# Kernel tuning notes

Measured on AMD Instinct MI355X. Metric: run time of the kernel, lower is better.

## Reference

```python
import jax, jax.numpy as jnp
import numpy as np

EPS = 1e-5

def conv3d(x, w):
    # x: [B,C,D,H,W], w: [O,I,3,3,3], stride 1, padding 1 (size preserving)
    return jax.lax.conv_general_dilated(
        x, w, window_strides=(1, 1, 1),
        padding=((1, 1), (1, 1), (1, 1)),
        dimension_numbers=('NCDHW', 'OIDHW', 'NCDHW'))

def deconv3d(x, w):
    # ConvTranspose3d(k=3, s=1, p=1) == conv3d with spatially flipped kernel, in/out swapped
    # torch ConvTranspose3d weight layout: [in, out, kD, kH, kW]
    wc = jnp.flip(w, axis=(2, 3, 4)).transpose(1, 0, 2, 3, 4)
    return conv3d(x, wc)

def batchnorm(x, bn):
    # bn: [4, C] rows = (gamma, beta, running_mean, running_var); inference mode
    g, b, m, v = bn[0], bn[1], bn[2], bn[3]
    scale = g * jax.lax.rsqrt(v + EPS)
    shift = b - m * scale
    return x * scale[None, :, None, None, None] + shift[None, :, None, None, None]

def qrnn_scan(Z, F, reverse):
    # gated linear recurrence h_t = f_t*h_{t-1} + (1-f_t)*z_t over depth axis (dim 2)
    Zs = jnp.moveaxis(Z, 2, 0)  # [D,B,C,H,W]
    Fs = jnp.moveaxis(F, 2, 0)
    def step(h, zf):
        z, f = zf
        h = f * h + (1.0 - f) * z
        return h, h
    h0 = jnp.zeros_like(Zs[0])  # h=None in torch == h=0 since f*0 vanishes
    _, hs = jax.lax.scan(step, h0, (Zs, Fs), reverse=reverse)
    return jnp.moveaxis(hs, 0, 2)

def qrnn_layer(x, w, bn, hidden, reverse, upsample, transpose):
    if upsample:
        # nn.Upsample(scale_factor=(1,2,2)) nearest
        x = jnp.repeat(jnp.repeat(x, 2, axis=3), 2, axis=4)
    g = deconv3d(x, w) if transpose else conv3d(x, w)
    g = batchnorm(g, bn)
    Z, F = g[:, :hidden], g[:, hidden:]
    return qrnn_scan(jnp.tanh(Z), jax.nn.sigmoid(F), reverse)

def setup_inputs():
    key = jax.random.key(0)
    ks = jax.random.split(key, 12)
    B, D = 4, 31
    x = jax.random.normal(ks[0], (B, 64, D, 32, 32), jnp.float32)
    xs2 = jax.random.normal(ks[1], (B, 32, D, 64, 64), jnp.float32)
    xs1 = jax.random.normal(ks[2], (B, 32, D, 64, 64), jnp.float32)
    xs0 = jax.random.normal(ks[3], (B, 16, D, 128, 128), jnp.float32)
    def wconv(k, shape):
        fan_in = shape[1] * 27
        return jax.random.normal(k, shape, jnp.float32) / np.float32(np.sqrt(fan_in))
    # layer0: UpsampleConv3d 64 -> 32 hidden (gates 64): Conv3d weight [64,64,3,3,3]
    w0 = wconv(ks[4], (64, 64, 3, 3, 3))
    # layer1: DeConv3D 32 -> 32 hidden (gates 64): ConvTranspose weight [in=32,out=64,3,3,3]
    w1 = wconv(ks[5], (32, 64, 3, 3, 3))
    # layer2: UpsampleConv3d 32 -> 16 hidden (gates 32): Conv3d weight [32,32,3,3,3]
    w2 = wconv(ks[6], (32, 32, 3, 3, 3))
    # layer3: DeConv3D 16 -> 16 hidden (gates 32): ConvTranspose weight [16,32,3,3,3]
    w3 = wconv(ks[7], (16, 32, 3, 3, 3))
    def mkbn(k, c):
        k1, k2, k3, k4 = jax.random.split(k, 4)
        return jnp.stack([
            jax.random.uniform(k1, (c,), jnp.float32, 0.5, 1.5),   # gamma
            jax.random.normal(k2, (c,), jnp.float32) * 0.1,        # beta
            jax.random.normal(k3, (c,), jnp.float32) * 0.1,        # running mean
            jax.random.uniform(k4, (c,), jnp.float32, 0.5, 1.5)])  # running var
    bn0 = mkbn(ks[8], 64)
    bn1 = mkbn(ks[9], 64)
    bn2 = mkbn(ks[10], 32)
    bn3 = mkbn(ks[11], 32)
    return dict(x=x, xs0=xs0, xs1=xs1, xs2=xs2,
                w0=w0, w1=w1, w2=w2, w3=w3,
                bn0=bn0, bn1=bn1, bn2=bn2, bn3=bn3)

def reference(x, xs0, xs1, xs2, w0, w1, w2, w3, bn0, bn1, bn2, bn3):
    # QRNN3DDecoder.forward with has_ad=True, reverse=False; scan direction alternates.
    # xs are popped last-first: xs2, xs1, xs0.
    h = qrnn_layer(x, w0, bn0, 32, False, True, False)          # upsample conv -> [B,32,D,64,64]
    h = qrnn_layer(h + xs2, w1, bn1, 32, True, False, True)     # deconv        -> [B,32,D,64,64]
    h = qrnn_layer(h + xs1, w2, bn2, 16, False, True, False)    # upsample conv -> [B,16,D,128,128]
    h = qrnn_layer(h + xs0, w3, bn3, 16, True, False, True)     # deconv        -> [B,16,D,128,128]
    return h
```

## Files before the change

### kernel.cpp

```cpp
#include <hip/hip_runtime.h>
#include <math.h>

#define BB 4
#define DD 31

typedef _Float16 half8 __attribute__((ext_vector_type(8)));
typedef float f32x4 __attribute__((ext_vector_type(4)));

__device__ __forceinline__ int swz(int b) { return b ^ (((b >> 7) & 7) << 4); }

__device__ __forceinline__ half8 ldswz(const _Float16* lin, int byteoff) {
    return *(const half8*)((const char*)lin + swz(byteoff));
}

__device__ __forceinline__ float fast_tanh(float y) {
    float e = __expf(2.f * y);
    return 1.f - 2.f * __builtin_amdgcn_rcpf(e + 1.f);
}
__device__ __forceinline__ float fast_sigmoid(float y) {
    return __builtin_amdgcn_rcpf(1.f + __expf(-y));
}


__global__ void bnprep(const float* __restrict__ bn, int C, float* __restrict__ sh) {
    int c = threadIdx.x;
    if (c >= C) return;
    float g = bn[c], b = bn[C + c], m = bn[2 * C + c], v = bn[3 * C + c];
    sh[c] = b - m * (g * rsqrtf(v + 1e-5f));
}

__global__ void wprep(const float* __restrict__ src, const float* __restrict__ bn,
                      _Float16* __restrict__ dst, int CIN, int COUT, int KS, int tr) {
    int idx = blockIdx.x * 256 + threadIdx.x;
    int total = KS * 32 * COUT;
    if (idx >= total) return;
    int ki = idx % 32;
    int co = (idx / 32) % COUT;
    int ko = idx / (32 * COUT);
    int k = ko * 32 + ki;
    float v = 0.f;
    if (k < 27 * CIN) {
        int tap = k / CIN, ci = k % CIN;
        v = tr ? src[((size_t)ci * COUT + co) * 27 + (26 - tap)]
               : src[((size_t)co * CIN + ci) * 27 + tap];
        v *= bn[co] * rsqrtf(bn[3 * COUT + co] + 1e-5f);
    }
    dst[((size_t)ko * COUT + co) * 32 + ki] = (_Float16)v;
}

__global__ void wprep_up(const float* __restrict__ src, const float* __restrict__ bn,
                         _Float16* __restrict__ dst, int CIN, int COUT) {
    const int KS = 12 * CIN / 32;
    int idx = blockIdx.x * 256 + threadIdx.x;
    int total = 4 * KS * 32 * COUT;
    if (idx >= total) return;
    int ki = idx % 32;
    int co = (idx / 32) % COUT;
    int ko = (idx / (32 * COUT)) % KS;
    int par = idx / (32 * COUT * KS);
    int k = ko * 32 + ki;
    int ci = k % CIN, tap = k / CIN;
    int kd = tap >> 2, ih = (tap >> 1) & 1, iw = tap & 1;
    int ph = par >> 1, pw = par & 1;
    const float c[2][2][3] = {{{1, 0, 0}, {0, 1, 1}}, {{1, 1, 0}, {0, 0, 1}}};
    float v = 0.f;
    for (int kh = 0; kh < 3; ++kh)
        for (int kw = 0; kw < 3; ++kw)
            v += c[ph][ih][kh] * c[pw][iw][kw] *
                 src[((size_t)co * CIN + ci) * 27 + kd * 9 + kh * 3 + kw];
    v *= bn[co] * rsqrtf(bn[3 * COUT + co] + 1e-5f);
    dst[(((size_t)par * KS + ko) * COUT + co) * 32 + ki] = (_Float16)v;
}

__global__ __launch_bounds__(256) void xconv(const float* __restrict__ src,
                                             _Float16* __restrict__ dst) {
    int idx = blockIdx.x * 256 + threadIdx.x;
    if (idx >= 4 * 31 * 1024 * 8) return;
    int cb = idx & 7;
    int pos = (idx >> 3) & 1023;
    int bd = idx >> 13;
    int d = bd % 31, b = bd / 31;
    half8 v;
#pragma unroll
    for (int j = 0; j < 8; ++j)
        v[j] = (_Float16)src[(((size_t)b * 64 + cb * 8 + j) * 31 + d) * 1024 + pos];
    *(half8*)(dst + ((size_t)bd * 1024 + pos) * 64 + cb * 8) = v;
}

template <int CIN, int COUT, int S, int KSTEPS>
__global__ __launch_bounds__(256, 2) void conv_mfma(
    const _Float16* __restrict__ inp,
    const _Float16* __restrict__ wq,
    const float* __restrict__ bnsh,
    _Float16* __restrict__ gout) {

    constexpr int IH = 18;
    constexpr int IW = 18;
    constexpr int NCB = COUT / 16;
    constexpr int NC8 = CIN / 8;
    constexpr int PATCH = 3 * IH * IW;

    __shared__ __align__(16) _Float16 lin[PATCH * CIN];

    const int tid = threadIdx.x;
    const int lane = tid & 63;
    const int wv = tid >> 6;
    const int col = lane & 15;
    const int grp = lane >> 4;

    const int w0 = blockIdx.x * 16;
    const int h0 = blockIdx.y * 16;
    const int bz = blockIdx.z;
    const int d = bz % DD;

    const int ibh = h0 - 1;
    const int ibw = w0 - 1;

    for (int idx = tid; idx < PATCH * NC8; idx += 256) {
        int c8 = idx % NC8;
        int pos = idx / NC8;
        int iw = pos % IW, t = pos / IW;
        int ih = t % IH, kd = t / IH;
        int dz = d + kd - 1, gh = ibh + ih, gw = ibw + iw;
        half8 v = {0, 0, 0, 0, 0, 0, 0, 0};
        if ((unsigned)dz < (unsigned)DD && (unsigned)gh < (unsigned)S &&
            (unsigned)gw < (unsigned)S)
            v = *(const half8*)(inp +
                (((size_t)(bz + kd - 1) * S + gh) * S + gw) * CIN + c8 * 8);
        *(half8*)((char*)lin + swz((pos * CIN + c8 * 8) * 2)) = v;
    }
    __syncthreads();

    f32x4 acc[4][NCB];
#pragma unroll
    for (int f = 0; f < 4; ++f)
#pragma unroll
        for (int n = 0; n < NCB; ++n) acc[f][n] = {0.f, 0.f, 0.f, 0.f};

#pragma unroll
    for (int ko = 0; ko < KSTEPS; ++ko) {
        int kd, kh, kw, ci;
        if (CIN >= 32) {
            int tap = (ko * 32) / CIN;
            kd = tap / 9; kh = (tap / 3) % 3; kw = tap % 3;
            ci = (ko * 32) % CIN + grp * 8;
        } else {
            int t0 = (2 * ko < 27) ? 2 * ko : 26;
            int t1 = (2 * ko + 1 < 27) ? 2 * ko + 1 : 26;
            int hi = grp >> 1;
            kd = hi ? t1 / 9 : t0 / 9;
            kh = hi ? (t1 / 3) % 3 : (t0 / 3) % 3;
            kw = hi ? t1 % 3 : t0 % 3;
            ci = (grp & 1) * 8;
        }

        half8 a[4];
        int iw = col + kw;
        int cb = ((kd * IH + wv * 4 + kh) * IW + iw) * CIN + ci;
#pragma unroll
        for (int f = 0; f < 4; ++f)
            a[f] = ldswz(lin, (cb + f * IW * CIN) * 2);

        half8 bfr[NCB];
#pragma unroll
        for (int n = 0; n < NCB; ++n)
            bfr[n] = *(const half8*)(wq + ((ko * COUT + n * 16 + col) * 32 + grp * 8));
#pragma unroll
        for (int f = 0; f < 4; ++f)
#pragma unroll
            for (int n = 0; n < NCB; ++n)
                acc[f][n] = __builtin_amdgcn_mfma_f32_16x16x32_f16(a[f], bfr[n],
                                                                   acc[f][n], 0, 0, 0);
    }

    const size_t obase = (size_t)bz * S * S * COUT;
#pragma unroll
    for (int n = 0; n < NCB; ++n) {
        int co = n * 16 + col;
        float sh = bnsh[co];
#pragma unroll
        for (int f = 0; f < 4; ++f) {
            int h = h0 + wv * 4 + f;
#pragma unroll
            for (int r = 0; r < 4; ++r) {
                int w = w0 + grp * 4 + r;
                float y = acc[f][n][r] + sh;
                float v = (n < NCB / 2) ? fast_tanh(y) : fast_sigmoid(y);
                gout[obase + ((size_t)h * S + w) * COUT + co] = (_Float16)v;
            }
        }
    }
}

template <int CIN, int COUT, int S, int MINW>
__global__ __launch_bounds__(256, MINW) void conv_up(
    const _Float16* __restrict__ inp,
    const _Float16* __restrict__ wqu,
    const float* __restrict__ bnsh,
    _Float16* __restrict__ gout) {

    constexpr int SIN = S / 2;
    constexpr int KS = 12 * CIN / 32;
    constexpr int NCB = COUT / 16;
    constexpr int NC8 = CIN / 8;
    constexpr int IH = 6, IW = 18;
    constexpr int PATCH = 3 * IH * IW;

    __shared__ __align__(16) _Float16 lin[PATCH * CIN];

    const int tid = threadIdx.x;
    const int lane = tid & 63;
    const int wv = tid >> 6;
    const int col = lane & 15;
    const int grp = lane >> 4;
    const int ph = wv >> 1, pw = wv & 1;

    const int bwp = blockIdx.x * 16;
    const int bhp = blockIdx.y * 4;
    const int bz = blockIdx.z;
    const int d = bz % DD;

    for (int idx = tid; idx < PATCH * NC8; idx += 256) {
        int c8 = idx % NC8;
        int pos = idx / NC8;
        int iwp = pos % IW, t = pos / IW;
        int ihp = t % IH, kd = t / IH;
        int dz = d + kd - 1, gh = bhp - 1 + ihp, gw = bwp - 1 + iwp;
        half8 v = {0, 0, 0, 0, 0, 0, 0, 0};
        if ((unsigned)dz < (unsigned)DD && (unsigned)gh < (unsigned)SIN &&
            (unsigned)gw < (unsigned)SIN)
            v = *(const half8*)(inp +
                (((size_t)(bz + kd - 1) * SIN + gh) * SIN + gw) * CIN + c8 * 8);
        *(half8*)((char*)lin + swz((pos * CIN + c8 * 8) * 2)) = v;
    }
    __syncthreads();

    f32x4 acc[4][NCB];
#pragma unroll
    for (int f = 0; f < 4; ++f)
#pragma unroll
        for (int n = 0; n < NCB; ++n) acc[f][n] = {0.f, 0.f, 0.f, 0.f};

    const _Float16* wqp = wqu + (size_t)(ph * 2 + pw) * KS * COUT * 32;

#pragma unroll
    for (int ko = 0; ko < KS; ++ko) {
        int tap = (ko * 32) / CIN;
        int ci = (ko * 32) % CIN + grp * 8;
        int kd = tap >> 2, ih = (tap >> 1) & 1, iwk = tap & 1;

        int lcol = col + iwk + pw;
        int r0 = ih + ph;
        int cb = ((kd * IH + r0) * IW + lcol) * CIN + ci;
        half8 a[4];
#pragma unroll
        for (int f = 0; f < 4; ++f)
            a[f] = ldswz(lin, (cb + f * IW * CIN) * 2);

        half8 bfr[NCB];
#pragma unroll
        for (int n = 0; n < NCB; ++n)
            bfr[n] = *(const half8*)(wqp + ((ko * COUT + n * 16 + col) * 32 + grp * 8));
#pragma unroll
        for (int f = 0; f < 4; ++f)
#pragma unroll
            for (int n = 0; n < NCB; ++n)
                acc[f][n] = __builtin_amdgcn_mfma_f32_16x16x32_f16(a[f], bfr[n],
                                                                   acc[f][n], 0, 0, 0);
    }

    const size_t obase = (size_t)bz * S * S * COUT;
#pragma unroll
    for (int n = 0; n < NCB; ++n) {
        int co = n * 16 + col;
        float sh = bnsh[co];
#pragma unroll
        for (int f = 0; f < 4; ++f) {
            int h = 2 * (bhp + f) + ph;
#pragma unroll
            for (int r = 0; r < 4; ++r) {
                int w = 2 * (bwp + grp * 4 + r) + pw;
                float y = acc[f][n][r] + sh;
                float v = (n < NCB / 2) ? fast_tanh(y) : fast_sigmoid(y);
                gout[obase + ((size_t)h * S + w) * COUT + co] = (_Float16)v;
            }
        }
    }
}

template <int H, int HW, int LAST>
__global__ __launch_bounds__(256) void qscan(
    const _Float16* __restrict__ g, const float* __restrict__ xs,
    _Float16* __restrict__ hout, float* __restrict__ fout, int rev) {
    constexpr int NCB = H / 8;
    int idx = blockIdx.x * 256 + threadIdx.x;
    if (idx >= BB * HW * NCB) return;
    int cb = idx % NCB;
    int hw = (idx / NCB) % HW;
    int b = idx / (NCB * HW);
    int c0 = cb * 8;

    float h[8];
#pragma unroll
    for (int j = 0; j < 8; ++j) h[j] = 0.f;

    for (int t = 0; t < DD; ++t) {
        int d = rev ? (DD - 1 - t) : t;
        const _Float16* gp = g + ((size_t)(b * DD + d) * HW + hw) * (2 * H);
        half8 z8 = *(const half8*)(gp + c0);
        half8 f8 = *(const half8*)(gp + H + c0);
        if (LAST) {
#pragma unroll
            for (int j = 0; j < 8; ++j) {
                float fv = (float)f8[j];
                h[j] = fv * h[j] + (1.f - fv) * (float)z8[j];
                fout[(((size_t)b * H + c0 + j) * DD + d) * HW + hw] = h[j];
            }
        } else {
            half8 o;
#pragma unroll
            for (int j = 0; j < 8; ++j) {
                float fv = (float)f8[j];
                h[j] = fv * h[j] + (1.f - fv) * (float)z8[j];
                o[j] = (_Float16)(h[j] + xs[(((size_t)b * H + c0 + j) * DD + d) * HW + hw]);
            }
            *(half8*)(hout + ((size_t)(b * DD + d) * HW + hw) * H + c0) = o;
        }
    }
}

extern "C" void kernel_launch(void* const* d_in, const int* in_sizes, int n_in,
                              void* d_out, int out_size, void* d_ws, size_t ws_size,
                              hipStream_t stream) {
    const float* x   = (const float*)d_in[0];
    const float* xs0 = (const float*)d_in[1];
    const float* xs1 = (const float*)d_in[2];
    const float* xs2 = (const float*)d_in[3];
    const float* w0  = (const float*)d_in[4];
    const float* w1  = (const float*)d_in[5];
    const float* w2  = (const float*)d_in[6];
    const float* w3  = (const float*)d_in[7];
    const float* bn0 = (const float*)d_in[8];
    const float* bn1 = (const float*)d_in[9];
    const float* bn2 = (const float*)d_in[10];
    const float* bn3 = (const float*)d_in[11];
    float* out = (float*)d_out;

    char* p = (char*)d_ws;
    _Float16* xf = (_Float16*)p;  p += (size_t)124 * 1024 * 64 * 2;
    _Float16* gA = (_Float16*)p;  p += (size_t)124 * 4096 * 64 * 2;
    _Float16* hA = (_Float16*)p;  p += (size_t)124 * 4096 * 32 * 2;
    _Float16* gB = (_Float16*)p;  p += (size_t)124 * 16384 * 32 * 2;
    _Float16* hB = (_Float16*)p;  p += (size_t)124 * 16384 * 16 * 2;
    _Float16* wqu0 = (_Float16*)p; p += (size_t)4 * 24 * 64 * 32 * 2;
    _Float16* wq1  = (_Float16*)p; p += 27 * 64 * 32 * 2;
    _Float16* wqu2 = (_Float16*)p; p += (size_t)4 * 12 * 32 * 32 * 2;
    _Float16* wq3  = (_Float16*)p; p += 14 * 32 * 32 * 2;
    float* sh0 = (float*)p;       p += 64 * 4;
    float* sh1 = (float*)p;       p += 64 * 4;
    float* sh2 = (float*)p;       p += 64 * 4;
    float* sh3 = (float*)p;       p += 64 * 4;

    xconv<<<(4 * 31 * 1024 * 8 + 255) / 256, 256, 0, stream>>>(x, xf);
    wprep_up<<<(4 * 24 * 32 * 64 + 255) / 256, 256, 0, stream>>>(w0, bn0, wqu0, 64, 64);
    wprep<<<(27 * 32 * 64 + 255) / 256, 256, 0, stream>>>(w1, bn1, wq1, 32, 64, 27, 1);
    wprep_up<<<(4 * 12 * 32 * 32 + 255) / 256, 256, 0, stream>>>(w2, bn2, wqu2, 32, 32);
    wprep<<<(14 * 32 * 32 + 255) / 256, 256, 0, stream>>>(w3, bn3, wq3, 16, 32, 14, 1);
    bnprep<<<1, 64, 0, stream>>>(bn0, 64, sh0);
    bnprep<<<1, 64, 0, stream>>>(bn1, 64, sh1);
    bnprep<<<1, 64, 0, stream>>>(bn2, 32, sh2);
    bnprep<<<1, 64, 0, stream>>>(bn3, 32, sh3);

    conv_up<64, 64, 64, 3><<<dim3(2, 8, BB * DD), 256, 0, stream>>>(xf, wqu0, sh0, gA);
    qscan<32, 4096, 0><<<(BB * 4096 * 4 + 255) / 256, 256, 0, stream>>>(gA, xs2, hA, nullptr, 0);

    conv_mfma<32, 64, 64, 27><<<dim3(4, 4, BB * DD), 256, 0, stream>>>(hA, wq1, sh1, gA);
    qscan<32, 4096, 0><<<(BB * 4096 * 4 + 255) / 256, 256, 0, stream>>>(gA, xs1, hA, nullptr, 1);

    conv_up<32, 32, 128, 4><<<dim3(4, 16, BB * DD), 256, 0, stream>>>(hA, wqu2, sh2, gB);
    qscan<16, 16384, 0><<<(BB * 16384 * 2 + 255) / 256, 256, 0, stream>>>(gB, xs0, hB, nullptr, 0);

    conv_mfma<16, 32, 128, 14><<<dim3(8, 8, BB * DD), 256, 0, stream>>>(hB, wq3, sh3, gB);
    qscan<16, 16384, 1><<<(BB * 16384 * 2 + 255) / 256, 256, 0, stream>>>(gB, nullptr, nullptr, out, 1);
}
```

Measured before the change: 567.1 us.

## Fuse conv, gating and depth scan for the two full-resolution layers

The last two layers become persistent kernels. Each block walks the depth axis in order, computes the conv with MFMA for one slice, applies tanh/sigmoid and updates the recurrence in registers. This removes the large fp16 gate tensors gB and their separate scan passes. Weights stay in registers, and input planes are kept in a rolling three-slice buffer (registers for the upsample layer, LDS for the last deconv). Parallelism drops to a grid over spatial tiles only, with the depth dimension serial, which risks low occupancy and latency-bound execution. xs0 is also converted to fp16 channel-last ahead of time.

Measured after the change: 522.0 us. 1.09x faster.

```diff
diff --git a/kernel.cpp b/kernel.cpp
--- a/kernel.cpp
+++ b/kernel.cpp
@@ -8,11 +8,12 @@
 typedef float f32x4 __attribute__((ext_vector_type(4)));
 
 __device__ __forceinline__ int swz(int b) { return b ^ (((b >> 7) & 7) << 4); }
-
 __device__ __forceinline__ half8 ldswz(const _Float16* lin, int byteoff) {
     return *(const half8*)((const char*)lin + swz(byteoff));
 }
-
+__device__ __forceinline__ void stswz(_Float16* lin, int byteoff, half8 v) {
+    *(half8*)((char*)lin + swz(byteoff)) = v;
+}
 __device__ __forceinline__ float fast_tanh(float y) {
     float e = __expf(2.f * y);
     return 1.f - 2.f * __builtin_amdgcn_rcpf(e + 1.f);
@@ -29,8 +30,8 @@
     sh[c] = b - m * (g * rsqrtf(v + 1e-5f));
 }
 
-__global__ void wprep(const float* __restrict__ src, const float* __restrict__ bn,
-                      _Float16* __restrict__ dst, int CIN, int COUT, int KS, int tr) {
+__global__ void wprepA(const float* __restrict__ src, const float* __restrict__ bn,
+                       _Float16* __restrict__ dst, int CIN, int COUT, int KS, int tr) {
     int idx = blockIdx.x * 256 + threadIdx.x;
     int total = KS * 32 * COUT;
     if (idx >= total) return;
@@ -48,8 +49,29 @@
     dst[((size_t)ko * COUT + co) * 32 + ki] = (_Float16)v;
 }
 
-__global__ void wprep_up(const float* __restrict__ src, const float* __restrict__ bn,
-                         _Float16* __restrict__ dst, int CIN, int COUT) {
+__global__ void wprepC(const float* __restrict__ src, const float* __restrict__ bn,
+                       _Float16* __restrict__ dst, int CIN, int COUT, int KS, int tr) {
+    int idx = blockIdx.x * 256 + threadIdx.x;
+    int total = KS * 1024;
+    if (idx >= total) return;
+    int ki = idx & 31;
+    int c16 = (idx >> 5) & 15;
+    int n = (idx >> 9) & 1;
+    int ko = idx >> 10;
+    int co = n * (COUT / 2) + c16;
+    int k = ko * 32 + ki;
+    float v = 0.f;
+    if (k < 27 * CIN) {
+        int tap = k / CIN, ci = k % CIN;
+        v = tr ? src[((size_t)ci * COUT + co) * 27 + (26 - tap)]
+               : src[((size_t)co * CIN + ci) * 27 + tap];
+        v *= bn[co] * rsqrtf(bn[3 * COUT + co] + 1e-5f);
+    }
+    dst[idx] = (_Float16)v;
+}
+
+__global__ void wprep_upA(const float* __restrict__ src, const float* __restrict__ bn,
+                          _Float16* __restrict__ dst, int CIN, int COUT) {
     const int KS = 12 * CIN / 32;
     int idx = blockIdx.x * 256 + threadIdx.x;
     int total = 4 * KS * 32 * COUT;
@@ -72,6 +94,31 @@
     dst[(((size_t)par * KS + ko) * COUT + co) * 32 + ki] = (_Float16)v;
 }
 
+__global__ void wprep_upB(const float* __restrict__ src, const float* __restrict__ bn,
+                          _Float16* __restrict__ dst, int CIN, int COUT, int KS) {
+    int idx = blockIdx.x * 256 + threadIdx.x;
+    int total = 4 * KS * 1024;
+    if (idx >= total) return;
+    int ki = idx & 31;
+    int c16 = (idx >> 5) & 15;
+    int n = (idx >> 9) & 1;
+    int ko = (idx >> 10) % KS;
+    int par = idx / (KS * 1024);
+    int co = n * (COUT / 2) + c16;
+    int k = ko * 32 + ki;
+    int ci = k % CIN, tap = k / CIN;
+    int kd = tap >> 2, ih = (tap >> 1) & 1, iw = tap & 1;
+    int ph = par >> 1, pw = par & 1;
+    const float c[2][2][3] = {{{1, 0, 0}, {0, 1, 1}}, {{1, 1, 0}, {0, 0, 1}}};
+    float v = 0.f;
+    for (int kh = 0; kh < 3; ++kh)
+        for (int kw = 0; kw < 3; ++kw)
+            v += c[ph][ih][kh] * c[pw][iw][kw] *
+                 src[((size_t)co * CIN + ci) * 27 + kd * 9 + kh * 3 + kw];
+    v *= bn[co] * rsqrtf(bn[3 * COUT + co] + 1e-5f);
+    dst[idx] = (_Float16)v;
+}
+
 __global__ __launch_bounds__(256) void xconv(const float* __restrict__ src,
                                              _Float16* __restrict__ dst) {
     int idx = blockIdx.x * 256 + threadIdx.x;
@@ -87,13 +134,118 @@
     *(half8*)(dst + ((size_t)bd * 1024 + pos) * 64 + cb * 8) = v;
 }
 
+template <int C, int HW>
+__global__ __launch_bounds__(256) void xst(const float* __restrict__ src,
+                                           _Float16* __restrict__ dst) {
+    int hw = blockIdx.x * 256 + threadIdx.x;
+    int bd = blockIdx.y;
+    int d = bd % DD, b = bd / DD;
+    _Float16 tmp[C];
+#pragma unroll
+    for (int c = 0; c < C; ++c)
+        tmp[c] = (_Float16)src[((size_t)(b * C + c) * DD + d) * HW + hw];
+#pragma unroll
+    for (int c8 = 0; c8 < C / 8; ++c8)
+        *(half8*)(dst + ((size_t)bd * HW + hw) * C + c8 * 8) = *(half8*)(tmp + c8 * 8);
+}
+
+template <int CIN, int COUT, int S, int MINW>
+__global__ __launch_bounds__(256, MINW) void conv_up(
+    const _Float16* __restrict__ inp, const _Float16* __restrict__ wqu,
+    const float* __restrict__ bnsh, _Float16* __restrict__ gout) {
+    constexpr int SIN = S / 2;
+    constexpr int KS = 12 * CIN / 32;
+    constexpr int NCB = COUT / 16;
+    constexpr int NC8 = CIN / 8;
+    constexpr int IH = 6, IW = 18;
+    constexpr int PATCH = 3 * IH * IW;
+
+    __shared__ __align__(16) _Float16 lin[PATCH * CIN];
+
+    const int tid = threadIdx.x;
+    const int lane = tid & 63;
+    const int wv = tid >> 6;
+    const int col = lane & 15;
+    const int grp = lane >> 4;
+    const int ph = wv >> 1, pw = wv & 1;
+
+    const int bwp = blockIdx.x * 16;
+    const int bhp = blockIdx.y * 4;
+    const int bz = blockIdx.z;
+    const int d = bz % DD;
+
+    for (int idx = tid; idx < PATCH * NC8; idx += 256) {
+        int c8 = idx % NC8;
+        int pos = idx / NC8;
+        int iwp = pos % IW, t = pos / IW;
+        int ihp = t % IH, kd = t / IH;
+        int dz = d + kd - 1, gh = bhp - 1 + ihp, gw = bwp - 1 + iwp;
+        half8 v = {0, 0, 0, 0, 0, 0, 0, 0};
+        if ((unsigned)dz < (unsigned)DD && (unsigned)gh < (unsigned)SIN &&
+            (unsigned)gw < (unsigned)SIN)
+            v = *(const half8*)(inp +
+                (((size_t)(bz + kd - 1) * SIN + gh) * SIN + gw) * CIN + c8 * 8);
+        *(half8*)((char*)lin + swz((pos * CIN + c8 * 8) * 2)) = v;
+    }
+    __syncthreads();
+
+    f32x4 acc[4][NCB];
+#pragma unroll
+    for (int f = 0; f < 4; ++f)
+#pragma unroll
+        for (int n = 0; n < NCB; ++n) acc[f][n] = {0.f, 0.f, 0.f, 0.f};
+
+    const _Float16* wqp = wqu + (size_t)(ph * 2 + pw) * KS * COUT * 32;
+
+#pragma unroll
+    for (int ko = 0; ko < KS; ++ko) {
+        int tap = (ko * 32) / CIN;
+        int ci = (ko * 32) % CIN + grp * 8;
+        int kd = tap >> 2, ih = (tap >> 1) & 1, iwk = tap & 1;
+
+        int lcol = col + iwk + pw;
+        int r0 = ih + ph;
+        int cb = ((kd * IH + r0) * IW + lcol) * CIN + ci;
+        half8 a[4];
+#pragma unroll
+        for (int f = 0; f < 4; ++f)
+            a[f] = ldswz(lin, (cb + f * IW * CIN) * 2);
+
+        half8 bfr[NCB];
+#pragma unroll
+        for (int n = 0; n < NCB; ++n)
+            bfr[n] = *(const half8*)(wqp + ((ko * COUT + n * 16 + col) * 32 + grp * 8));
+#pragma unroll
+        for (int f = 0; f < 4; ++f)
+#pragma unroll
+            for (int n = 0; n < NCB; ++n)
+                acc[f][n] = __builtin_amdgcn_mfma_f32_16x16x32_f16(a[f], bfr[n],
+                                                                   acc[f][n], 0, 0, 0);
+    }
+
+    const size_t obase = (size_t)bz * S * S * COUT;
+#pragma unroll
+    for (int n = 0; n < NCB; ++n) {
+        int co = n * 16 + col;
+        float sh = bnsh[co];
+#pragma unroll
+        for (int f = 0; f < 4; ++f) {
+            int h = 2 * (bhp + f) + ph;
+#pragma unroll
+            for (int r = 0; r < 4; ++r) {
+                int w = 2 * (bwp + grp * 4 + r) + pw;
+                float y = acc[f][n][r] + sh;
+                float v = (n < NCB / 2) ? fast_tanh(y) : fast_sigmoid(y);
+                gout[obase + ((size_t)h * S + w) * COUT + co] = (_Float16)v;
+            }
+        }
+    }
+}
+
 template <int CIN, int COUT, int S, int KSTEPS>
 __global__ __launch_bounds__(256, 2) void conv_mfma(
-    const _Float16* __restrict__ inp,
-    const _Float16* __restrict__ wq,
-    const float* __restrict__ bnsh,
-    _Float16* __restrict__ gout) {
-
+    const _Float16* __restrict__ inp, const _Float16* __restrict__ wq,
+    const float* __restrict__ bnsh, _Float16* __restrict__ gout) {
     constexpr int IH = 18;
     constexpr int IW = 18;
     constexpr int NCB = COUT / 16;
@@ -139,20 +291,9 @@
 
 #pragma unroll
     for (int ko = 0; ko < KSTEPS; ++ko) {
-        int kd, kh, kw, ci;
-        if (CIN >= 32) {
-            int tap = (ko * 32) / CIN;
-            kd = tap / 9; kh = (tap / 3) % 3; kw = tap % 3;
-            ci = (ko * 32) % CIN + grp * 8;
-        } else {
-            int t0 = (2 * ko < 27) ? 2 * ko : 26;
-            int t1 = (2 * ko + 1 < 27) ? 2 * ko + 1 : 26;
-            int hi = grp >> 1;
-            kd = hi ? t1 / 9 : t0 / 9;
-            kh = hi ? (t1 / 3) % 3 : (t0 / 3) % 3;
-            kw = hi ? t1 % 3 : t0 % 3;
-            ci = (grp & 1) * 8;
-        }
+        int tap = (ko * 32) / CIN;
+        int kd = tap / 9, kh = (tap / 3) % 3, kw = tap % 3;
+        int ci = (ko * 32) % CIN + grp * 8;
 
         half8 a[4];
         int iw = col + kw;
@@ -192,106 +333,10 @@
     }
 }
 
-template <int CIN, int COUT, int S, int MINW>
-__global__ __launch_bounds__(256, MINW) void conv_up(
-    const _Float16* __restrict__ inp,
-    const _Float16* __restrict__ wqu,
-    const float* __restrict__ bnsh,
-    _Float16* __restrict__ gout) {
-
-    constexpr int SIN = S / 2;
-    constexpr int KS = 12 * CIN / 32;
-    constexpr int NCB = COUT / 16;
-    constexpr int NC8 = CIN / 8;
-    constexpr int IH = 6, IW = 18;
-    constexpr int PATCH = 3 * IH * IW;
-
-    __shared__ __align__(16) _Float16 lin[PATCH * CIN];
-
-    const int tid = threadIdx.x;
-    const int lane = tid & 63;
-    const int wv = tid >> 6;
-    const int col = lane & 15;
-    const int grp = lane >> 4;
-    const int ph = wv >> 1, pw = wv & 1;
-
-    const int bwp = blockIdx.x * 16;
-    const int bhp = blockIdx.y * 4;
-    const int bz = blockIdx.z;
-    const int d = bz % DD;
-
-    for (int idx = tid; idx < PATCH * NC8; idx += 256) {
-        int c8 = idx % NC8;
-        int pos = idx / NC8;
-        int iwp = pos % IW, t = pos / IW;
-        int ihp = t % IH, kd = t / IH;
-        int dz = d + kd - 1, gh = bhp - 1 + ihp, gw = bwp - 1 + iwp;
-        half8 v = {0, 0, 0, 0, 0, 0, 0, 0};
-        if ((unsigned)dz < (unsigned)DD && (unsigned)gh < (unsigned)SIN &&
-            (unsigned)gw < (unsigned)SIN)
-            v = *(const half8*)(inp +
-                (((size_t)(bz + kd - 1) * SIN + gh) * SIN + gw) * CIN + c8 * 8);
-        *(half8*)((char*)lin + swz((pos * CIN + c8 * 8) * 2)) = v;
-    }
-    __syncthreads();
-
-    f32x4 acc[4][NCB];
-#pragma unroll
-    for (int f = 0; f < 4; ++f)
-#pragma unroll
-        for (int n = 0; n < NCB; ++n) acc[f][n] = {0.f, 0.f, 0.f, 0.f};
-
-    const _Float16* wqp = wqu + (size_t)(ph * 2 + pw) * KS * COUT * 32;
-
-#pragma unroll
-    for (int ko = 0; ko < KS; ++ko) {
-        int tap = (ko * 32) / CIN;
-        int ci = (ko * 32) % CIN + grp * 8;
-        int kd = tap >> 2, ih = (tap >> 1) & 1, iwk = tap & 1;
-
-        int lcol = col + iwk + pw;
-        int r0 = ih + ph;
-        int cb = ((kd * IH + r0) * IW + lcol) * CIN + ci;
-        half8 a[4];
-#pragma unroll
-        for (int f = 0; f < 4; ++f)
-            a[f] = ldswz(lin, (cb + f * IW * CIN) * 2);
-
-        half8 bfr[NCB];
-#pragma unroll
-        for (int n = 0; n < NCB; ++n)
-            bfr[n] = *(const half8*)(wqp + ((ko * COUT + n * 16 + col) * 32 + grp * 8));
-#pragma unroll
-        for (int f = 0; f < 4; ++f)
-#pragma unroll
-            for (int n = 0; n < NCB; ++n)
-                acc[f][n] = __builtin_amdgcn_mfma_f32_16x16x32_f16(a[f], bfr[n],
-                                                                   acc[f][n], 0, 0, 0);
-    }
-
-    const size_t obase = (size_t)bz * S * S * COUT;
-#pragma unroll
-    for (int n = 0; n < NCB; ++n) {
-        int co = n * 16 + col;
-        float sh = bnsh[co];
-#pragma unroll
-        for (int f = 0; f < 4; ++f) {
-            int h = 2 * (bhp + f) + ph;
-#pragma unroll
-            for (int r = 0; r < 4; ++r) {
-                int w = 2 * (bwp + grp * 4 + r) + pw;
-                float y = acc[f][n][r] + sh;
-                float v = (n < NCB / 2) ? fast_tanh(y) : fast_sigmoid(y);
-                gout[obase + ((size_t)h * S + w) * COUT + co] = (_Float16)v;
-            }
-        }
-    }
-}
-
-template <int H, int HW, int LAST>
+template <int H, int HW>
 __global__ __launch_bounds__(256) void qscan(
     const _Float16* __restrict__ g, const float* __restrict__ xs,
-    _Float16* __restrict__ hout, float* __restrict__ fout, int rev) {
+    _Float16* __restrict__ hout, int rev) {
     constexpr int NCB = H / 8;
     int idx = blockIdx.x * 256 + threadIdx.x;
     if (idx >= BB * HW * NCB) return;
@@ -309,24 +354,228 @@
         const _Float16* gp = g + ((size_t)(b * DD + d) * HW + hw) * (2 * H);
         half8 z8 = *(const half8*)(gp + c0);
         half8 f8 = *(const half8*)(gp + H + c0);
-        if (LAST) {
-#pragma unroll
-            for (int j = 0; j < 8; ++j) {
-                float fv = (float)f8[j];
-                h[j] = fv * h[j] + (1.f - fv) * (float)z8[j];
-                fout[(((size_t)b * H + c0 + j) * DD + d) * HW + hw] = h[j];
-            }
+        half8 o;
+#pragma unroll
+        for (int j = 0; j < 8; ++j) {
+            float fv = (float)f8[j];
+            h[j] = fv * h[j] + (1.f - fv) * (float)z8[j];
+            o[j] = (_Float16)(h[j] + xs[(((size_t)b * H + c0 + j) * DD + d) * HW + hw]);
+        }
+        *(half8*)(hout + ((size_t)(b * DD + d) * HW + hw) * H + c0) = o;
+    }
+}
+
+__global__ __launch_bounds__(256, 2) void fup3(
+    const _Float16* __restrict__ inp,
+    const _Float16* __restrict__ wq,
+    const float* __restrict__ bnsh,
+    const _Float16* __restrict__ xs,
+    _Float16* __restrict__ hout) {
+    constexpr int CIN = 32, S = 128, SIN = 64, HID = 16, KS = 12;
+
+    const int tid = threadIdx.x, lane = tid & 63, wv = tid >> 6;
+    const int col = lane & 15, grp = lane >> 4;
+    const int bwp = blockIdx.x * 16, bhp = blockIdx.y * 4;
+    const int par = blockIdx.z & 3, b = blockIdx.z >> 2;
+    const int ph = par >> 1, pw = par & 1;
+    const size_t bbase = (size_t)b * DD;
+
+    half8 wz[KS], wf[KS];
+    {
+        const _Float16* wqb = wq + (size_t)par * KS * 1024 + col * 32 + grp * 8;
+#pragma unroll
+        for (int ko = 0; ko < KS; ++ko) {
+            wz[ko] = *(const half8*)(wqb + ko * 1024);
+            wf[ko] = *(const half8*)(wqb + ko * 1024 + 512);
+        }
+    }
+
+    const int gh0 = bhp - 1 + wv + ph;
+    const int gw0 = bwp - 1 + col + pw;
+    const bool vr0 = (unsigned)gh0 < (unsigned)SIN, vr1 = (unsigned)(gh0 + 1) < (unsigned)SIN;
+    const bool vc0 = (unsigned)gw0 < (unsigned)SIN, vc1 = (unsigned)(gw0 + 1) < (unsigned)SIN;
+    const int o00 = (gh0 * SIN + gw0) * CIN + grp * 8;
+    const int o01 = o00 + CIN;
+    const int o10 = o00 + SIN * CIN;
+    const int o11 = o10 + CIN;
+    const half8 Z8 = {0, 0, 0, 0, 0, 0, 0, 0};
+
+    half8 A[2][2], Bp[2][2], Cp[2][2];
+
+    auto ldp = [&](int dz, half8 (&P)[2][2]) {
+        if ((unsigned)dz < (unsigned)DD) {
+            const _Float16* pl = inp + (bbase + dz) * (size_t)(SIN * SIN * CIN);
+            P[0][0] = (vr0 && vc0) ? *(const half8*)(pl + o00) : Z8;
+            P[0][1] = (vr0 && vc1) ? *(const half8*)(pl + o01) : Z8;
+            P[1][0] = (vr1 && vc0) ? *(const half8*)(pl + o10) : Z8;
+            P[1][1] = (vr1 && vc1) ? *(const half8*)(pl + o11) : Z8;
         } else {
-            half8 o;
-#pragma unroll
-            for (int j = 0; j < 8; ++j) {
-                float fv = (float)f8[j];
-                h[j] = fv * h[j] + (1.f - fv) * (float)z8[j];
-                o[j] = (_Float16)(h[j] + xs[(((size_t)b * H + c0 + j) * DD + d) * HW + hw]);
-            }
-            *(half8*)(hout + ((size_t)(b * DD + d) * HW + hw) * H + c0) = o;
-        }
-    }
+            P[0][0] = Z8; P[0][1] = Z8; P[1][0] = Z8; P[1][1] = Z8;
+        }
+    };
+
+    ldp(-1, A);
+    ldp(0, Bp);
+    ldp(1, Cp);
+
+    float hst[4] = {0.f, 0.f, 0.f, 0.f};
+    const float shz = bnsh[col];
+    const float shf = bnsh[HID + col];
+    const int h = 2 * (bhp + wv) + ph;
+    const int wr = 2 * (bwp + grp * 4) + pw;
+
+    auto body = [&](int d, half8 (&PA)[2][2], half8 (&PB)[2][2], half8 (&PC)[2][2]) {
+        f32x4 az = {0.f, 0.f, 0.f, 0.f}, af = {0.f, 0.f, 0.f, 0.f};
+#pragma unroll
+        for (int ko = 0; ko < 4; ++ko) {
+            half8 a = PA[(ko >> 1) & 1][ko & 1];
+            az = __builtin_amdgcn_mfma_f32_16x16x32_f16(a, wz[ko], az, 0, 0, 0);
+            af = __builtin_amdgcn_mfma_f32_16x16x32_f16(a, wf[ko], af, 0, 0, 0);
+        }
+        ldp(d + 2, PA);
+#pragma unroll
+        for (int ko = 4; ko < 8; ++ko) {
+            half8 a = PB[(ko >> 1) & 1][ko & 1];
+            az = __builtin_amdgcn_mfma_f32_16x16x32_f16(a, wz[ko], az, 0, 0, 0);
+            af = __builtin_amdgcn_mfma_f32_16x16x32_f16(a, wf[ko], af, 0, 0, 0);
+        }
+#pragma unroll
+        for (int ko = 8; ko < 12; ++ko) {
+            half8 a = PC[(ko >> 1) & 1][ko & 1];
+            az = __builtin_amdgcn_mfma_f32_16x16x32_f16(a, wz[ko], az, 0, 0, 0);
+            af = __builtin_amdgcn_mfma_f32_16x16x32_f16(a, wf[ko], af, 0, 0, 0);
+        }
+        const size_t sb = (bbase + d) * (size_t)(S * S) + (size_t)h * S;
+#pragma unroll
+        for (int r = 0; r < 4; ++r) {
+            size_t sp = sb + wr + 2 * r;
+            float z = fast_tanh(az[r] + shz);
+            float fg = fast_sigmoid(af[r] + shf);
+            hst[r] = fg * hst[r] + (1.f - fg) * z;
+            float xv = (float)xs[sp * HID + col];
+            hout[sp * HID + col] = (_Float16)(hst[r] + xv);
+        }
+    };
+
+    for (int t = 0; t < 30; t += 3) {
+        body(t, A, Bp, Cp);
+        body(t + 1, Bp, Cp, A);
+        body(t + 2, Cp, A, Bp);
+    }
+    body(30, A, Bp, Cp);
+}
+
+__global__ __launch_bounds__(256, 2) void fdn4(
+    const _Float16* __restrict__ inp,
+    const _Float16* __restrict__ wq,
+    const float* __restrict__ bnsh,
+    float* __restrict__ fout) {
+    constexpr int CIN = 16, S = 128, HID = 16, KS = 14;
+    constexpr int SLOT = 1792;
+    __shared__ __align__(16) _Float16 lds[4 * 3 * SLOT / 2];
+
+    const int tid = threadIdx.x, lane = tid & 63, wv = tid >> 6;
+    const int col = lane & 15, grp = lane >> 4;
+    const int w0 = blockIdx.x * 16, h0 = blockIdx.y * 4;
+    const int b = blockIdx.z;
+    const size_t bbase = (size_t)b * DD;
+    const int wvbase = wv * 3 * SLOT;
+    const int hi = grp >> 1, cih = (grp & 1) * 8;
+    const half8 Z8 = {0, 0, 0, 0, 0, 0, 0, 0};
+
+    half8 wz[KS], wf[KS];
+    {
+        const _Float16* wqb = wq + col * 32 + grp * 8;
+#pragma unroll
+        for (int ko = 0; ko < KS; ++ko) {
+            wz[ko] = *(const half8*)(wqb + ko * 1024);
+            wf[ko] = *(const half8*)(wqb + ko * 1024 + 512);
+        }
+    }
+
+    auto ldchunk = [&](int dz, int idx) -> half8 {
+        int r = idx / 36, rem = idx - r * 36;
+        int c = rem >> 1, g = rem & 1;
+        int gh = h0 - 1 + wv + r, gw = w0 - 1 + c;
+        if ((unsigned)dz < (unsigned)DD && (unsigned)gh < (unsigned)S &&
+            (unsigned)gw < (unsigned)S)
+            return *(const half8*)(inp + (((bbase + dz) * S + gh) * S + gw) * CIN + g * 8);
+        return Z8;
+    };
+    auto wrchunk = [&](int sbyte, int idx, half8 v) {
+        int r = idx / 36, rem = idx - r * 36;
+        int c = rem >> 1, g = rem & 1;
+        stswz(lds, wvbase + sbyte + ((r * 18 + c) * 16 + g * 8) * 2, v);
+    };
+    auto stage = [&](int dz, int sbyte) {
+        half8 v0 = ldchunk(dz, lane);
+        wrchunk(sbyte, lane, v0);
+        if (lane < 44) {
+            half8 v1 = ldchunk(dz, lane + 64);
+            wrchunk(sbyte, lane + 64, v1);
+        }
+    };
+
+    stage(29, 0);
+    stage(30, SLOT);
+    stage(31, 2 * SLOT);
+
+    float hst[4] = {0.f, 0.f, 0.f, 0.f};
+    const float shz = bnsh[col];
+    const float shf = bnsh[HID + col];
+
+    auto body = [&](int d, int sA, int sB, int sC) {
+        half8 sv0 = ldchunk(d - 2, lane);
+        half8 sv1 = (lane < 44) ? ldchunk(d - 2, lane + 64) : Z8;
+
+        f32x4 az = {0.f, 0.f, 0.f, 0.f}, af = {0.f, 0.f, 0.f, 0.f};
+#pragma unroll
+        for (int ko = 9; ko < 14; ++ko) {
+            const int t0 = (2 * ko < 27) ? 2 * ko : 26;
+            const int t1 = (2 * ko + 1 < 27) ? 2 * ko + 1 : 26;
+            const int off0 = (((t0 / 3) % 3) * 18 + col + t0 % 3) * 32 + cih * 2;
+            const int off1 = (((t1 / 3) % 3) * 18 + col + t1 % 3) * 32 + cih * 2;
+            int ab = wvbase + sC + (hi ? off1 : off0);
+            half8 a = ldswz(lds, ab);
+            az = __builtin_amdgcn_mfma_f32_16x16x32_f16(a, wz[ko], az, 0, 0, 0);
+            af = __builtin_amdgcn_mfma_f32_16x16x32_f16(a, wf[ko], af, 0, 0, 0);
+        }
+#pragma unroll
+        for (int ko = 0; ko < 9; ++ko) {
+            const int t0 = 2 * ko;
+            const int t1 = 2 * ko + 1;
+            const int sK0 = (t0 / 9 == 0) ? 0 : 1;
+            const int sK1 = (t1 / 9 == 0) ? 0 : 1;
+            const int off0 = (((t0 / 3) % 3) * 18 + col + t0 % 3) * 32 + cih * 2;
+            const int off1 = (((t1 / 3) % 3) * 18 + col + t1 % 3) * 32 + cih * 2;
+            int a0 = (sK0 ? sB : sA) + off0;
+            int a1 = (sK1 ? sB : sA) + off1;
+            int ab = wvbase + (hi ? a1 : a0);
+            half8 a = ldswz(lds, ab);
+            az = __builtin_amdgcn_mfma_f32_16x16x32_f16(a, wz[ko], az, 0, 0, 0);
+            af = __builtin_amdgcn_mfma_f32_16x16x32_f16(a, wf[ko], af, 0, 0, 0);
+        }
+        wrchunk(sC, lane, sv0);
+        if (lane < 44) wrchunk(sC, lane + 64, sv1);
+
+        f32x4 o;
+#pragma unroll
+        for (int r = 0; r < 4; ++r) {
+            float z = fast_tanh(az[r] + shz);
+            float fg = fast_sigmoid(af[r] + shf);
+            hst[r] = fg * hst[r] + (1.f - fg) * z;
+            o[r] = hst[r];
+        }
+        *(f32x4*)(fout + (((size_t)b * HID + col) * DD + d) * (size_t)(S * S) +
+                  (size_t)(h0 + wv) * S + w0 + grp * 4) = o;
+    };
+
+    for (int t = 0; t < 30; t += 3) {
+        body(30 - t, 0, SLOT, 2 * SLOT);
+        body(29 - t, 2 * SLOT, 0, SLOT);
+        body(28 - t, SLOT, 2 * SLOT, 0);
+    }
+    body(0, 0, SLOT, 2 * SLOT);
 }
 
 extern "C" void kernel_launch(void* const* d_in, const int* in_sizes, int n_in,
@@ -347,39 +596,39 @@
     float* out = (float*)d_out;
 
     char* p = (char*)d_ws;
-    _Float16* xf = (_Float16*)p;  p += (size_t)124 * 1024 * 64 * 2;
-    _Float16* gA = (_Float16*)p;  p += (size_t)124 * 4096 * 64 * 2;
-    _Float16* hA = (_Float16*)p;  p += (size_t)124 * 4096 * 32 * 2;
-    _Float16* gB = (_Float16*)p;  p += (size_t)124 * 16384 * 32 * 2;
-    _Float16* hB = (_Float16*)p;  p += (size_t)124 * 16384 * 16 * 2;
-    _Float16* wqu0 = (_Float16*)p; p += (size_t)4 * 24 * 64 * 32 * 2;
-    _Float16* wq1  = (_Float16*)p; p += 27 * 64 * 32 * 2;
-    _Float16* wqu2 = (_Float16*)p; p += (size_t)4 * 12 * 32 * 32 * 2;
-    _Float16* wq3  = (_Float16*)p; p += 14 * 32 * 32 * 2;
-    float* sh0 = (float*)p;       p += 64 * 4;
-    float* sh1 = (float*)p;       p += 64 * 4;
-    float* sh2 = (float*)p;       p += 64 * 4;
-    float* sh3 = (float*)p;       p += 64 * 4;
+    _Float16* xf   = (_Float16*)p; p += (size_t)124 * 1024 * 64 * 2;
+    _Float16* gA   = (_Float16*)p; p += (size_t)124 * 4096 * 64 * 2;
+    _Float16* hA   = (_Float16*)p; p += (size_t)124 * 4096 * 32 * 2;
+    _Float16* hA2  = (_Float16*)p; p += (size_t)124 * 4096 * 32 * 2;
+    _Float16* hB   = (_Float16*)p; p += (size_t)124 * 16384 * 16 * 2;
+    _Float16* xs0f = (_Float16*)p; p += (size_t)124 * 16384 * 16 * 2;
+    _Float16* wq0u = (_Float16*)p; p += (size_t)4 * 24 * 64 * 32 * 2;
+    _Float16* wq1  = (_Float16*)p; p += (size_t)27 * 64 * 32 * 2;
+    _Float16* wq2u = (_Float16*)p; p += (size_t)4 * 12 * 1024 * 2;
+    _Float16* wq3  = (_Float16*)p; p += (size_t)14 * 1024 * 2;
+    float* sh0 = (float*)p; p += 64 * 4;
+    float* sh1 = (float*)p; p += 64 * 4;
+    float* sh2 = (float*)p; p += 64 * 4;
+    float* sh3 = (float*)p; p += 64 * 4;
 
     xconv<<<(4 * 31 * 1024 * 8 + 255) / 256, 256, 0, stream>>>(x, xf);
-    wprep_up<<<(4 * 24 * 32 * 64 + 255) / 256, 256, 0, stream>>>(w0, bn0, wqu0, 64, 64);
-    wprep<<<(27 * 32 * 64 + 255) / 256, 256, 0, stream>>>(w1, bn1, wq1, 32, 64, 27, 1);
-    wprep_up<<<(4 * 12 * 32 * 32 + 255) / 256, 256, 0, stream>>>(w2, bn2, wqu2, 32, 32);
-    wprep<<<(14 * 32 * 32 + 255) / 256, 256, 0, stream>>>(w3, bn3, wq3, 16, 32, 14, 1);
+    xst<16, 16384><<<dim3(64, BB * DD), 256, 0, stream>>>(xs0, xs0f);
+    wprep_upA<<<(4 * 24 * 32 * 64 + 255) / 256, 256, 0, stream>>>(w0, bn0, wq0u, 64, 64);
+    wprepA<<<(27 * 32 * 64 + 255) / 256, 256, 0, stream>>>(w1, bn1, wq1, 32, 64, 27, 1);
+    wprep_upB<<<(4 * 12 * 1024 + 255) / 256, 256, 0, stream>>>(w2, bn2, wq2u, 32, 32, 12);
+    wprepC<<<(14 * 1024 + 255) / 256, 256, 0, stream>>>(w3, bn3, wq3, 16, 32, 14, 1);
     bnprep<<<1, 64, 0, stream>>>(bn0, 64, sh0);
     bnprep<<<1, 64, 0, stream>>>(bn1, 64, sh1);
     bnprep<<<1, 64, 0, stream>>>(bn2, 32, sh2);
     bnprep<<<1, 64, 0, stream>>>(bn3, 32, sh3);
 
-    conv_up<64, 64, 64, 3><<<dim3(2, 8, BB * DD), 256, 0, stream>>>(xf, wqu0, sh0, gA);
-    qscan<32, 4096, 0><<<(BB * 4096 * 4 + 255) / 256, 256, 0, stream>>>(gA, xs2, hA, nullptr, 0);
+    conv_up<64, 64, 64, 3><<<dim3(2, 8, BB * DD), 256, 0, stream>>>(xf, wq0u, sh0, gA);
+    qscan<32, 4096><<<(BB * 4096 * 4 + 255) / 256, 256, 0, stream>>>(gA, xs2, hA, 0);
 
     conv_mfma<32, 64, 64, 27><<<dim3(4, 4, BB * DD), 256, 0, stream>>>(hA, wq1, sh1, gA);
-    qscan<32, 4096, 0><<<(BB * 4096 * 4 + 255) / 256, 256, 0, stream>>>(gA, xs1, hA, nullptr, 1);
-
-    conv_up<32, 32, 128, 4><<<dim3(4, 16, BB * DD), 256, 0, stream>>>(hA, wqu2, sh2, gB);
-    qscan<16, 16384, 0><<<(BB * 16384 * 2 + 255) / 256, 256, 0, stream>>>(gB, xs0, hB, nullptr, 0);
-
-    conv_mfma<16, 32, 128, 14><<<dim3(8, 8, BB * DD), 256, 0, stream>>>(hB, wq3, sh3, gB);
-    qscan<16, 16384, 1><<<(BB * 16384 * 2 + 255) / 256, 256, 0, stream>>>(gB, nullptr, nullptr, out, 1);
-}
+    qscan<32, 4096><<<(BB * 4096 * 4 + 255) / 256, 256, 0, stream>>>(gA, xs1, hA2, 1);
+
+    fup3<<<dim3(4, 16, BB * 4), 256, 0, stream>>>(hA2, wq2u, sh2, xs0f, hB);
+
+    fdn4<<<dim3(8, 32, BB), 256, 0, stream>>>(hB, wq3, sh3, out);
+}
```
